# Optimization experiments

Hardware: AMD Instinct MI355X
Metric: run time of the kernel (lower is better)

The kernel has to match this reference:

```python
import jax, jax.numpy as jnp
import numpy as np

NUM_CODES = 100000
NUM_EDGES = 20000
DIM = 128
DEG = 32  # nodes per hyperedge -> 640000 incidences


def setup_inputs() -> dict:
    key = jax.random.key(0)
    k1, k2, k3, k4, k5 = jax.random.split(key, 5)
    n_inc = NUM_EDGES * DEG
    # incidence list: edge_ids is sorted (CSR-style), node_ids are member nodes
    node_ids = jax.random.randint(k1, (n_inc,), 0, NUM_CODES, dtype=jnp.int32)
    edge_ids = jnp.repeat(jnp.arange(NUM_EDGES, dtype=jnp.int32), DEG)
    # learned parameters (xavier-ish scales)
    node_emb = jax.random.normal(k2, (NUM_CODES, DIM), jnp.float32) * (1.0 / np.sqrt(DIM))
    edge_emb = jax.random.normal(k3, (NUM_EDGES, DIM), jnp.float32) * (1.0 / np.sqrt(DIM))
    W_e = jax.random.normal(k4, (DIM, DIM), jnp.float32) * (1.0 / np.sqrt(DIM))
    b_e = jnp.zeros((DIM,), jnp.float32)
    W_v = jax.random.normal(k5, (DIM, DIM), jnp.float32) * (1.0 / np.sqrt(DIM))
    b_v = jnp.zeros((DIM,), jnp.float32)
    return {"node_emb": node_emb, "edge_emb": edge_emb, "W_e": W_e, "b_e": b_e,
            "W_v": W_v, "b_v": b_v, "node_ids": node_ids, "edge_ids": edge_ids}


def reference(node_emb, edge_emb, W_e, b_e, W_v, b_v, node_ids, edge_ids):
    N, D = node_emb.shape
    E = edge_emb.shape[0]
    # node -> edge: mean of member node embeddings per hyperedge (segment mean)
    gathered = node_emb[node_ids]                                    # [I, D]
    seg_sum = jax.ops.segment_sum(gathered, edge_ids, num_segments=E)  # [E, D]
    seg_cnt = jax.ops.segment_sum(jnp.ones_like(edge_ids, jnp.float32), edge_ids, num_segments=E)
    mean = seg_sum / jnp.maximum(seg_cnt, 1.0)[:, None]
    # empty edges fall back to their own edge embedding (as in the torch loop)
    edge_ctx = jnp.where(seg_cnt[:, None] > 0, mean, edge_emb)
    edge_ctx = edge_ctx @ W_e.T + b_e                                # lin_e
    # edge -> node: scatter-add edge_ctx back to member nodes
    node_sum = jnp.zeros_like(node_emb).at[node_ids].add(edge_ctx[edge_ids])
    deg = jnp.zeros((N,), jnp.float32).at[node_ids].add(1.0)
    node_cnt = 1.0 + deg  # torch code clamps zeros to 1 BEFORE adding counts
    node_ctx = (node_sum / node_cnt[:, None]) @ W_v.T + b_v          # lin_v
    node_out = node_emb + node_ctx
    edge_out = edge_emb + edge_ctx
    return (node_out, edge_out)
```

## Files before the change

### kernel.cpp

```cpp
#include <hip/hip_runtime.h>

#define DIMS 128
#define DEG 32
#define CAP 32

typedef __attribute__((ext_vector_type(8))) short short8;
typedef __attribute__((ext_vector_type(4))) float floatx4;

static __device__ __forceinline__ unsigned short f2bf(float f) {
  unsigned int u = __float_as_uint(f);
  unsigned int r = (u + 0x7FFFu + ((u >> 16) & 1u)) >> 16;
  return (unsigned short)r;
}
static __device__ __forceinline__ float bf2f(unsigned short v) {
  return __uint_as_float(((unsigned int)v) << 16);
}

__global__ __launch_bounds__(256) void k_cvt_all(
    const float* __restrict__ a0, unsigned short* __restrict__ d0, int n0,
    const float* __restrict__ a1, unsigned short* __restrict__ d1, int n1,
    int* __restrict__ cnt, int ncnt) {
  int t = blockIdx.x * 256 + threadIdx.x;
  if (t < ncnt) cnt[t] = 0;
  int i = t * 4;
  const float* s; unsigned short* d;
  if (i < n0) { s = a0 + i; d = d0 + i; }
  else if (i < n0 + n1) { s = a1 + (i - n0); d = d1 + (i - n0); }
  else return;
  float4 v = *(const float4*)s;
  ushort4 o;
  o.x = f2bf(v.x); o.y = f2bf(v.y); o.z = f2bf(v.z); o.w = f2bf(v.w);
  *(ushort4*)d = o;
}

__global__ __launch_bounds__(256) void k_prep_wc(
    const float* __restrict__ Wv, const float* __restrict__ We,
    const float* __restrict__ be,
    unsigned short* __restrict__ Wc, float* __restrict__ bc) {
  int tid = threadIdx.x;
  if (blockIdx.x == 16) {
    __shared__ float be_s[DIMS];
    if (tid < DIMS) be_s[tid] = be[tid];
    __syncthreads();
    if (tid < DIMS) {
      float s = 0.f;
      for (int c = 0; c < DIMS; ++c) s += Wv[(size_t)tid * DIMS + c] * be_s[c];
      bc[tid] = s;
    }
    return;
  }
  __shared__ __align__(16) float We_s[DIMS][DIMS];
  __shared__ __align__(16) float wv_s[8][DIMS];
  int d0 = blockIdx.x * 8;
#pragma unroll
  for (int u = 0; u < 16; ++u) {
    int idx = tid + u * 256;
    int row = idx >> 5, c4 = idx & 31;
    *(float4*)&We_s[row][c4 * 4] = ((const float4*)We)[idx];
  }
  {
    int row = tid >> 5, c4 = tid & 31;
    *(float4*)&wv_s[row][c4 * 4] = ((const float4*)(Wv + (size_t)d0 * DIMS))[tid];
  }
  __syncthreads();
  int dd = tid >> 5;
  int k4 = (tid & 31) * 4;
  float4 acc = {0.f, 0.f, 0.f, 0.f};
  for (int c = 0; c < DIMS; ++c) {
    float w = wv_s[dd][c];
    float4 we = *(const float4*)&We_s[c][k4];
    acc.x += w * we.x; acc.y += w * we.y; acc.z += w * we.z; acc.w += w * we.w;
  }
  ushort4 o;
  o.x = f2bf(acc.x); o.y = f2bf(acc.y); o.z = f2bf(acc.z); o.w = f2bf(acc.w);
  *(ushort4*)(Wc + (size_t)(d0 + dd) * DIMS + k4) = o;
}

__global__ __launch_bounds__(256) void k_edge_mean_fill(
    const unsigned short* __restrict__ node_emb_bf,
    const int* __restrict__ node_ids,
    unsigned short* __restrict__ mean_bf,
    int* __restrict__ cnt,
    unsigned short* __restrict__ bucket,
    int E) {
  int e0 = blockIdx.x * 16;
  int tid = threadIdx.x;
  __shared__ int ids[16][DEG];
#pragma unroll
  for (int u = 0; u < 2; ++u) {
    int idx = tid + u * 256;
    int ee = idx >> 5, j = idx & 31;
    int e = e0 + ee;
    ids[ee][j] = (e < E) ? node_ids[(size_t)e * DEG + j] : 0;
  }
  __syncthreads();
  int ee = tid >> 4;
  int l8 = tid & 15;
  int e = e0 + ee;
  if (e < E) {
    float acc[8] = {0.f, 0.f, 0.f, 0.f, 0.f, 0.f, 0.f, 0.f};
#pragma unroll
    for (int jb = 0; jb < DEG; jb += 8) {
      short8 v[8];
#pragma unroll
      for (int u = 0; u < 8; ++u) {
        int n = ids[ee][jb + u];
        v[u] = *(const short8*)(node_emb_bf + (size_t)n * DIMS + l8 * 8);
      }
#pragma unroll
      for (int u = 0; u < 8; ++u)
#pragma unroll
        for (int t = 0; t < 8; ++t) acc[t] += bf2f((unsigned short)v[u][t]);
    }
    const float s = 1.0f / (float)DEG;
    short8 o;
#pragma unroll
    for (int t = 0; t < 8; ++t) o[t] = (short)f2bf(acc[t] * s);
    *(short8*)(mean_bf + (size_t)e * DIMS + l8 * 8) = o;
  }
#pragma unroll
  for (int u = 0; u < 2; ++u) {
    int idx = tid + u * 256;
    int ee2 = idx >> 5;
    int e2 = e0 + ee2;
    if (e2 < E) {
      int n = ids[ee2][idx & 31];
      int pos = atomicAdd(&cnt[n], 1);
      if (pos < CAP) bucket[(size_t)n * CAP + pos] = (unsigned short)e2;
    }
  }
}

__global__ __launch_bounds__(256) void k_gemm_dual(
    const unsigned short* __restrict__ X,
    const unsigned short* __restrict__ We,
    const unsigned short* __restrict__ Wc,
    const float* __restrict__ be,
    const float* __restrict__ bc,
    const float* __restrict__ edge_emb,
    float* __restrict__ edge_out,
    unsigned short* __restrict__ ectx2,
    int R) {
  int tid = threadIdx.x;
  int wave = tid >> 6;
  int lane = tid & 63;
  int ln = lane & 15;
  int quad = lane >> 4;
  int r0 = (blockIdx.x * 4 + wave) * 16;

  int r = r0 + ln;
  int rc = (r < R) ? r : (R - 1);

  floatx4 acc_e[8], acc_c[8];
#pragma unroll
  for (int tm = 0; tm < 8; ++tm) {
    acc_e[tm] = (floatx4){0.f, 0.f, 0.f, 0.f};
    acc_c[tm] = (floatx4){0.f, 0.f, 0.f, 0.f};
  }

#pragma unroll
  for (int kc = 0; kc < 4; ++kc) {
    int kb = kc * 32 + quad * 8;
    short8 a = *(const short8*)(X + (size_t)rc * DIMS + kb);
#pragma unroll
    for (int tm = 0; tm < 8; ++tm) {
      short8 bwe = *(const short8*)(We + (size_t)(tm * 16 + ln) * DIMS + kb);
      short8 bwc = *(const short8*)(Wc + (size_t)(tm * 16 + ln) * DIMS + kb);
      acc_e[tm] = __builtin_amdgcn_mfma_f32_16x16x32_bf16(bwe, a, acc_e[tm], 0, 0, 0);
      acc_c[tm] = __builtin_amdgcn_mfma_f32_16x16x32_bf16(bwc, a, acc_c[tm], 0, 0, 0);
    }
  }

  int rE = r0 + ln;
  if (rE >= R) return;
#pragma unroll
  for (int tm = 0; tm < 8; ++tm) {
    int c0 = tm * 16 + quad * 4;
    size_t off = (size_t)rE * DIMS + c0;
    float4 bev = *(const float4*)(be + c0);
    float4 rv = *(const float4*)(edge_emb + off);
    float4 ve;
    ve.x = acc_e[tm][0] + bev.x + rv.x;
    ve.y = acc_e[tm][1] + bev.y + rv.y;
    ve.z = acc_e[tm][2] + bev.z + rv.z;
    ve.w = acc_e[tm][3] + bev.w + rv.w;
    *(float4*)(edge_out + off) = ve;

    float4 bcv = *(const float4*)(bc + c0);
    ushort4 oc;
    oc.x = f2bf(acc_c[tm][0] + bcv.x);
    oc.y = f2bf(acc_c[tm][1] + bcv.y);
    oc.z = f2bf(acc_c[tm][2] + bcv.z);
    oc.w = f2bf(acc_c[tm][3] + bcv.w);
    *(ushort4*)(ectx2 + off) = oc;
  }
}

__global__ __launch_bounds__(256) void k_node_out(
    const unsigned short* __restrict__ ectx2,
    const unsigned short* __restrict__ bucket,
    const int* __restrict__ cnt,
    const unsigned short* __restrict__ node_emb_bf,
    const float* __restrict__ bv,
    float* __restrict__ node_out,
    int N) {
  int n0 = blockIdx.x * 16;
  int tid = threadIdx.x;
  __shared__ unsigned short elist[16][CAP];
  __shared__ float scale_s[16];
  __shared__ int cnt_s[16];
  {
    int nn = tid >> 4, p = tid & 15;
    int n = n0 + nn;
    unsigned int v = (n < N)
        ? ((const unsigned int*)(bucket + (size_t)n * CAP))[p] : 0u;
    elist[nn][p * 2] = (unsigned short)(v & 0xFFFFu);
    elist[nn][p * 2 + 1] = (unsigned short)(v >> 16);
  }
  if (tid < 16) {
    int n = n0 + tid;
    int c = (n < N) ? cnt[n] : 0;
    scale_s[tid] = 1.0f / (1.0f + (float)c);
    cnt_s[tid] = c > CAP ? CAP : c;
  }
  __syncthreads();
  int nn = tid >> 4;
  int l8 = tid & 15;
  int n = n0 + nn;
  if (n >= N) return;
  int c = cnt_s[nn];
  float acc[8] = {0.f, 0.f, 0.f, 0.f, 0.f, 0.f, 0.f, 0.f};
  int j = 0;
  for (; j + 4 <= c; j += 4) {
    short8 v0 = *(const short8*)(ectx2 + (size_t)elist[nn][j + 0] * DIMS + l8 * 8);
    short8 v1 = *(const short8*)(ectx2 + (size_t)elist[nn][j + 1] * DIMS + l8 * 8);
    short8 v2 = *(const short8*)(ectx2 + (size_t)elist[nn][j + 2] * DIMS + l8 * 8);
    short8 v3 = *(const short8*)(ectx2 + (size_t)elist[nn][j + 3] * DIMS + l8 * 8);
#pragma unroll
    for (int t = 0; t < 8; ++t)
      acc[t] += bf2f((unsigned short)v0[t]) + bf2f((unsigned short)v1[t]) +
                bf2f((unsigned short)v2[t]) + bf2f((unsigned short)v3[t]);
  }
  for (; j < c; ++j) {
    short8 v = *(const short8*)(ectx2 + (size_t)elist[nn][j] * DIMS + l8 * 8);
#pragma unroll
    for (int t = 0; t < 8; ++t) acc[t] += bf2f((unsigned short)v[t]);
  }
  float sc = scale_s[nn];
  short8 rb = *(const short8*)(node_emb_bf + (size_t)n * DIMS + l8 * 8);
  float4 bv0 = *(const float4*)(bv + l8 * 8);
  float4 bv1 = *(const float4*)(bv + l8 * 8 + 4);
  float4 o0, o1;
  o0.x = acc[0] * sc + bf2f((unsigned short)rb[0]) + bv0.x;
  o0.y = acc[1] * sc + bf2f((unsigned short)rb[1]) + bv0.y;
  o0.z = acc[2] * sc + bf2f((unsigned short)rb[2]) + bv0.z;
  o0.w = acc[3] * sc + bf2f((unsigned short)rb[3]) + bv0.w;
  o1.x = acc[4] * sc + bf2f((unsigned short)rb[4]) + bv1.x;
  o1.y = acc[5] * sc + bf2f((unsigned short)rb[5]) + bv1.y;
  o1.z = acc[6] * sc + bf2f((unsigned short)rb[6]) + bv1.z;
  o1.w = acc[7] * sc + bf2f((unsigned short)rb[7]) + bv1.w;
  float* dst = node_out + (size_t)n * DIMS + l8 * 8;
  *(float4*)dst = o0;
  *(float4*)(dst + 4) = o1;
}

extern "C" void kernel_launch(void* const* d_in, const int* in_sizes, int n_in,
                              void* d_out, int out_size, void* d_ws, size_t ws_size,
                              hipStream_t stream) {
  const float* node_emb = (const float*)d_in[0];
  const float* edge_emb = (const float*)d_in[1];
  const float* W_e      = (const float*)d_in[2];
  const float* b_e      = (const float*)d_in[3];
  const float* W_v      = (const float*)d_in[4];
  const float* b_v      = (const float*)d_in[5];
  const int*   node_ids = (const int*)d_in[6];

  const int N = in_sizes[0] / DIMS;
  const int E = in_sizes[1] / DIMS;

  float* out      = (float*)d_out;
  float* node_out = out;
  float* edge_out = out + (size_t)N * DIMS;

  unsigned short* nb    = (unsigned short*)d_ws;
  unsigned short* meanb = nb + (size_t)N * DIMS;
  unsigned short* ectx2 = meanb + (size_t)E * DIMS;
  unsigned short* web   = ectx2 + (size_t)E * DIMS;
  unsigned short* wcb   = web + DIMS * DIMS;
  float* bc  = (float*)(wcb + DIMS * DIMS);
  int* cntb   = (int*)(bc + DIMS);
  unsigned short* bucket = (unsigned short*)(cntb + N);

  int ntot = N * DIMS + DIMS * DIMS;
  k_cvt_all<<<(ntot / 4 + 255) / 256, 256, 0, stream>>>(
      node_emb, nb, N * DIMS, W_e, web, DIMS * DIMS, cntb, N);

  k_prep_wc<<<17, 256, 0, stream>>>(W_v, W_e, b_e, wcb, bc);

  k_edge_mean_fill<<<(E + 15) / 16, 256, 0, stream>>>(
      nb, node_ids, meanb, cntb, bucket, E);

  k_gemm_dual<<<(E + 63) / 64, 256, 0, stream>>>(
      meanb, web, wcb, b_e, bc, edge_emb, edge_out, ectx2, E);

  k_node_out<<<(N + 15) / 16, 256, 0, stream>>>(
      ectx2, bucket, cntb, nb, b_v, node_out, N);
}
```

Measured before the change: 216.3 us.

## Fuse edge segment-mean with dual edge GEMM through swizzled shared memory

Merges the edge mean/bucket-fill kernel and the dual MFMA GEMM kernel into one kernel. Each 16-edge block writes its bf16 means into an XOR-swizzled LDS tile, and its four waves then each compute 32 output columns with MFMA instead of each wave handling 16 rows across all 128 columns. This removes one kernel launch and the global write and read of the mean buffer. In exchange the weight rows are re-read from global or L2 by every block (1250 blocks instead of 313), and the GEMM work per wave is small.

```diff
diff --git a/kernel.cpp b/kernel.cpp
--- a/kernel.cpp
+++ b/kernel.cpp
@@ -76,63 +76,9 @@
   *(ushort4*)(Wc + (size_t)(d0 + dd) * DIMS + k4) = o;
 }
 
-__global__ __launch_bounds__(256) void k_edge_mean_fill(
+__global__ __launch_bounds__(256) void k_edge_fused(
     const unsigned short* __restrict__ node_emb_bf,
     const int* __restrict__ node_ids,
-    unsigned short* __restrict__ mean_bf,
-    int* __restrict__ cnt,
-    unsigned short* __restrict__ bucket,
-    int E) {
-  int e0 = blockIdx.x * 16;
-  int tid = threadIdx.x;
-  __shared__ int ids[16][DEG];
-#pragma unroll
-  for (int u = 0; u < 2; ++u) {
-    int idx = tid + u * 256;
-    int ee = idx >> 5, j = idx & 31;
-    int e = e0 + ee;
-    ids[ee][j] = (e < E) ? node_ids[(size_t)e * DEG + j] : 0;
-  }
-  __syncthreads();
-  int ee = tid >> 4;
-  int l8 = tid & 15;
-  int e = e0 + ee;
-  if (e < E) {
-    float acc[8] = {0.f, 0.f, 0.f, 0.f, 0.f, 0.f, 0.f, 0.f};
-#pragma unroll
-    for (int jb = 0; jb < DEG; jb += 8) {
-      short8 v[8];
-#pragma unroll
-      for (int u = 0; u < 8; ++u) {
-        int n = ids[ee][jb + u];
-        v[u] = *(const short8*)(node_emb_bf + (size_t)n * DIMS + l8 * 8);
-      }
-#pragma unroll
-      for (int u = 0; u < 8; ++u)
-#pragma unroll
-        for (int t = 0; t < 8; ++t) acc[t] += bf2f((unsigned short)v[u][t]);
-    }
-    const float s = 1.0f / (float)DEG;
-    short8 o;
-#pragma unroll
-    for (int t = 0; t < 8; ++t) o[t] = (short)f2bf(acc[t] * s);
-    *(short8*)(mean_bf + (size_t)e * DIMS + l8 * 8) = o;
-  }
-#pragma unroll
-  for (int u = 0; u < 2; ++u) {
-    int idx = tid + u * 256;
-    int ee2 = idx >> 5;
-    int e2 = e0 + ee2;
-    if (e2 < E) {
-      int n = ids[ee2][idx & 31];
-      int pos = atomicAdd(&cnt[n], 1);
-      if (pos < CAP) bucket[(size_t)n * CAP + pos] = (unsigned short)e2;
-    }
-  }
-}
-
-__global__ __launch_bounds__(256) void k_gemm_dual(
-    const unsigned short* __restrict__ X,
     const unsigned short* __restrict__ We,
     const unsigned short* __restrict__ Wc,
     const float* __restrict__ be,
@@ -140,58 +86,109 @@
     const float* __restrict__ edge_emb,
     float* __restrict__ edge_out,
     unsigned short* __restrict__ ectx2,
-    int R) {
+    int* __restrict__ cnt,
+    unsigned short* __restrict__ bucket,
+    int E) {
+  int e0 = blockIdx.x * 16;
   int tid = threadIdx.x;
+  __shared__ int ids[16][DEG];
+  __shared__ __align__(16) unsigned short xs[16 * DIMS];
+#pragma unroll
+  for (int u = 0; u < 2; ++u) {
+    int idx = tid + u * 256;
+    int ee = idx >> 5, j = idx & 31;
+    int e = e0 + ee;
+    ids[ee][j] = (e < E) ? node_ids[(size_t)e * DEG + j] : 0;
+  }
+  __syncthreads();
+
+  {
+    int ee = tid >> 4;
+    int l8 = tid & 15;
+    float acc[8] = {0.f, 0.f, 0.f, 0.f, 0.f, 0.f, 0.f, 0.f};
+#pragma unroll
+    for (int jb = 0; jb < DEG; jb += 8) {
+      short8 v[8];
+#pragma unroll
+      for (int u = 0; u < 8; ++u) {
+        int n = ids[ee][jb + u];
+        v[u] = *(const short8*)(node_emb_bf + (size_t)n * DIMS + l8 * 8);
+      }
+#pragma unroll
+      for (int u = 0; u < 8; ++u)
+#pragma unroll
+        for (int t = 0; t < 8; ++t) acc[t] += bf2f((unsigned short)v[u][t]);
+    }
+    const float s = 1.0f / (float)DEG;
+    short8 o;
+#pragma unroll
+    for (int t = 0; t < 8; ++t) o[t] = (short)f2bf(acc[t] * s);
+    int byt = ee * 256 + ((l8 * 16) ^ ((ee & 7) << 4));
+    *(short8*)((char*)xs + byt) = o;
+  }
+
+  {
+    int ia = tid, ib = tid + 256;
+    int ea = e0 + (ia >> 5), eb = e0 + (ib >> 5);
+    int na = ids[ia >> 5][ia & 31];
+    int nb = ids[ib >> 5][ib & 31];
+    int pa = CAP, pb = CAP;
+    bool va = ea < E, vb = eb < E;
+    if (va) pa = atomicAdd(&cnt[na], 1);
+    if (vb) pb = atomicAdd(&cnt[nb], 1);
+    if (va && pa < CAP) bucket[(size_t)na * CAP + pa] = (unsigned short)ea;
+    if (vb && pb < CAP) bucket[(size_t)nb * CAP + pb] = (unsigned short)eb;
+  }
+  __syncthreads();
+
   int wave = tid >> 6;
   int lane = tid & 63;
   int ln = lane & 15;
   int quad = lane >> 4;
-  int r0 = (blockIdx.x * 4 + wave) * 16;
-
-  int r = r0 + ln;
-  int rc = (r < R) ? r : (R - 1);
-
-  floatx4 acc_e[8], acc_c[8];
-#pragma unroll
-  for (int tm = 0; tm < 8; ++tm) {
-    acc_e[tm] = (floatx4){0.f, 0.f, 0.f, 0.f};
-    acc_c[tm] = (floatx4){0.f, 0.f, 0.f, 0.f};
-  }
+
+  floatx4 acc_e0 = {0.f,0.f,0.f,0.f}, acc_e1 = {0.f,0.f,0.f,0.f};
+  floatx4 acc_c0 = {0.f,0.f,0.f,0.f}, acc_c1 = {0.f,0.f,0.f,0.f};
 
 #pragma unroll
   for (int kc = 0; kc < 4; ++kc) {
+    int bofs = ln * 256 + ((kc * 64 + quad * 16) ^ ((ln & 7) << 4));
+    short8 a = *(const short8*)((const char*)xs + bofs);
     int kb = kc * 32 + quad * 8;
-    short8 a = *(const short8*)(X + (size_t)rc * DIMS + kb);
-#pragma unroll
-    for (int tm = 0; tm < 8; ++tm) {
-      short8 bwe = *(const short8*)(We + (size_t)(tm * 16 + ln) * DIMS + kb);
-      short8 bwc = *(const short8*)(Wc + (size_t)(tm * 16 + ln) * DIMS + kb);
-      acc_e[tm] = __builtin_amdgcn_mfma_f32_16x16x32_bf16(bwe, a, acc_e[tm], 0, 0, 0);
-      acc_c[tm] = __builtin_amdgcn_mfma_f32_16x16x32_bf16(bwc, a, acc_c[tm], 0, 0, 0);
-    }
-  }
-
-  int rE = r0 + ln;
-  if (rE >= R) return;
-#pragma unroll
-  for (int tm = 0; tm < 8; ++tm) {
-    int c0 = tm * 16 + quad * 4;
+    int wr0 = wave * 32 + ln;
+    int wr1 = wave * 32 + 16 + ln;
+    short8 bwe0 = *(const short8*)(We + (size_t)wr0 * DIMS + kb);
+    short8 bwc0 = *(const short8*)(Wc + (size_t)wr0 * DIMS + kb);
+    short8 bwe1 = *(const short8*)(We + (size_t)wr1 * DIMS + kb);
+    short8 bwc1 = *(const short8*)(Wc + (size_t)wr1 * DIMS + kb);
+    acc_e0 = __builtin_amdgcn_mfma_f32_16x16x32_bf16(bwe0, a, acc_e0, 0, 0, 0);
+    acc_c0 = __builtin_amdgcn_mfma_f32_16x16x32_bf16(bwc0, a, acc_c0, 0, 0, 0);
+    acc_e1 = __builtin_amdgcn_mfma_f32_16x16x32_bf16(bwe1, a, acc_e1, 0, 0, 0);
+    acc_c1 = __builtin_amdgcn_mfma_f32_16x16x32_bf16(bwc1, a, acc_c1, 0, 0, 0);
+  }
+
+  int rE = e0 + ln;
+  if (rE >= E) return;
+#pragma unroll
+  for (int t = 0; t < 2; ++t) {
+    floatx4 ae = t ? acc_e1 : acc_e0;
+    floatx4 ac = t ? acc_c1 : acc_c0;
+    int c0 = wave * 32 + t * 16 + quad * 4;
     size_t off = (size_t)rE * DIMS + c0;
     float4 bev = *(const float4*)(be + c0);
     float4 rv = *(const float4*)(edge_emb + off);
     float4 ve;
-    ve.x = acc_e[tm][0] + bev.x + rv.x;
-    ve.y = acc_e[tm][1] + bev.y + rv.y;
-    ve.z = acc_e[tm][2] + bev.z + rv.z;
-    ve.w = acc_e[tm][3] + bev.w + rv.w;
+    ve.x = ae[0] + bev.x + rv.x;
+    ve.y = ae[1] + bev.y + rv.y;
+    ve.z = ae[2] + bev.z + rv.z;
+    ve.w = ae[3] + bev.w + rv.w;
     *(float4*)(edge_out + off) = ve;
 
     float4 bcv = *(const float4*)(bc + c0);
     ushort4 oc;
-    oc.x = f2bf(acc_c[tm][0] + bcv.x);
-    oc.y = f2bf(acc_c[tm][1] + bcv.y);
-    oc.z = f2bf(acc_c[tm][2] + bcv.z);
-    oc.w = f2bf(acc_c[tm][3] + bcv.w);
+    oc.x = f2bf(ac[0] + bcv.x);
+    oc.y = f2bf(ac[1] + bcv.y);
+    oc.z = f2bf(ac[2] + bcv.z);
+    oc.w = f2bf(ac[3] + bcv.w);
     *(ushort4*)(ectx2 + off) = oc;
   }
 }
@@ -283,8 +280,7 @@
   float* edge_out = out + (size_t)N * DIMS;
 
   unsigned short* nb    = (unsigned short*)d_ws;
-  unsigned short* meanb = nb + (size_t)N * DIMS;
-  unsigned short* ectx2 = meanb + (size_t)E * DIMS;
+  unsigned short* ectx2 = nb + (size_t)N * DIMS;
   unsigned short* web   = ectx2 + (size_t)E * DIMS;
   unsigned short* wcb   = web + DIMS * DIMS;
   float* bc  = (float*)(wcb + DIMS * DIMS);
@@ -297,11 +293,9 @@
 
   k_prep_wc<<<17, 256, 0, stream>>>(W_v, W_e, b_e, wcb, bc);
 
-  k_edge_mean_fill<<<(E + 15) / 16, 256, 0, stream>>>(
-      nb, node_ids, meanb, cntb, bucket, E);
-
-  k_gemm_dual<<<(E + 63) / 64, 256, 0, stream>>>(
-      meanb, web, wcb, b_e, bc, edge_emb, edge_out, ectx2, E);
+  k_edge_fused<<<(E + 15) / 16, 256, 0, stream>>>(
+      nb, node_ids, web, wcb, b_e, bc, edge_emb, edge_out, ectx2,
+      cntb, bucket, E);
 
   k_node_out<<<(N + 15) / 16, 256, 0, stream>>>(
       ectx2, bucket, cntb, nb, b_v, node_out, N);
```

Result: faster. 200.1 us (-7.5%).
